# Kernel optimization log

Measured on AMD Instinct MI355X. Metric: run time of the kernel, lower is better.

The kernel has to match this reference:

```python
import jax, jax.numpy as jnp
import numpy as np

H = 768          # hidden_size
NH = 12          # num heads
HD = H // NH     # head dim = 64
FF = 4 * H       # 3072
EPS = 1e-12


def _layer_norm(x, g, b):
    mu = jnp.mean(x, axis=-1, keepdims=True)
    var = jnp.var(x, axis=-1, keepdims=True)
    return (x - mu) * jax.lax.rsqrt(var + EPS) * g + b


def setup_inputs() -> dict:
    key = jax.random.key(0)
    ks = jax.random.split(key, 8)
    B, S = 4, 2048
    s = 0.02
    return {
        "x": jax.random.normal(ks[0], (B, S, H), dtype=jnp.float32),
        "w_qkv": jax.random.normal(ks[1], (H, 3 * H), dtype=jnp.float32) * s,
        "b_qkv": jnp.zeros((3 * H,), dtype=jnp.float32),
        "w_out": jax.random.normal(ks[2], (H, H), dtype=jnp.float32) * s,
        "b_out": jnp.zeros((H,), dtype=jnp.float32),
        "w_ff1": jax.random.normal(ks[3], (H, FF), dtype=jnp.float32) * s,
        "b_ff1": jnp.zeros((FF,), dtype=jnp.float32),
        "w_ff2": jax.random.normal(ks[4], (FF, H), dtype=jnp.float32) * s,
        "b_ff2": jnp.zeros((H,), dtype=jnp.float32),
        "g1": jnp.ones((H,), dtype=jnp.float32),
        "be1": jnp.zeros((H,), dtype=jnp.float32),
        "g2": jnp.ones((H,), dtype=jnp.float32),
        "be2": jnp.zeros((H,), dtype=jnp.float32),
    }


def reference(x, w_qkv, b_qkv, w_out, b_out, w_ff1, b_ff1, w_ff2, b_ff2, g1, be1, g2, be2):
    B, S, _ = x.shape
    qkv = x @ w_qkv + b_qkv                     # [B,S,3H]
    q, k, v = jnp.split(qkv, 3, axis=-1)
    # [B,S,H] -> [B,NH,S,HD]
    def heads(t):
        return t.reshape(B, S, NH, HD).transpose(0, 2, 1, 3)
    q, k, v = heads(q), heads(k), heads(v)
    scores = jnp.einsum("bhqd,bhkd->bhqk", q, k) / np.sqrt(HD).astype(np.float32)
    attn = jax.nn.softmax(scores, axis=-1)      # dropout is identity at inference
    ctx = jnp.einsum("bhqk,bhkd->bhqd", attn, v)
    ctx = ctx.transpose(0, 2, 1, 3).reshape(B, S, H)
    attn_out = ctx @ w_out + b_out
    x1 = _layer_norm(x + attn_out, g1, be1)
    h = jax.nn.gelu(x1 @ w_ff1 + b_ff1, approximate=False)  # torch exact gelu
    ffn = h @ w_ff2 + b_ff2
    return _layer_norm(x1 + ffn, g2, be2)
```

## Files before the change

kernel.cpp:

```cpp
#include <hip/hip_runtime.h>
#include <cstdint>
#include <cstddef>

typedef unsigned short u16;
typedef __attribute__((ext_vector_type(8))) short bf16x8;
typedef __attribute__((ext_vector_type(4))) float f32x4;

__device__ __forceinline__ u16 f2b(float f) {
    union { float f; unsigned u; } un; un.f = f;
    unsigned r = un.u + 0x7fffu + ((un.u >> 16) & 1u);
    return (u16)(r >> 16);
}
__device__ __forceinline__ u16 f2b_trunc(float f) {
    union { float f; unsigned u; } un; un.f = f;
    return (u16)(un.u >> 16);
}
__device__ __forceinline__ float fast_exp2(float x) {
#if __has_builtin(__builtin_amdgcn_exp2f)
    return __builtin_amdgcn_exp2f(x);
#else
    return exp2f(x);
#endif
}

__device__ __forceinline__ void stage16(const u16* g, u16* l) {
    __builtin_amdgcn_global_load_lds(
        (const __attribute__((address_space(1))) void*)g,
        (__attribute__((address_space(3))) void*)l, 16, 0, 0);
}

__global__ __launch_bounds__(256) void cast_bf16_x4(const float* __restrict__ in,
                                                    u16* __restrict__ out, int n4) {
    int i = blockIdx.x * 256 + threadIdx.x;
    if (i >= n4) return;
    float4 v = ((const float4*)in)[i];
    ushort4 o;
    o.x = f2b(v.x); o.y = f2b(v.y); o.z = f2b(v.z); o.w = f2b(v.w);
    ((ushort4*)out)[i] = o;
}

__global__ __launch_bounds__(256) void transpose_cast(const float* __restrict__ in,
                                                      u16* __restrict__ out, int K, int N) {
    __shared__ float t[32][33];
    const int n0 = blockIdx.x * 32, k0 = blockIdx.y * 32;
    const int tx = threadIdx.x, ty = threadIdx.y;
#pragma unroll
    for (int i = 0; i < 4; ++i)
        t[ty + i * 8][tx] = in[(size_t)(k0 + ty + i * 8) * N + n0 + tx];
    __syncthreads();
#pragma unroll
    for (int i = 0; i < 4; ++i)
        out[(size_t)(n0 + ty + i * 8) * K + k0 + tx] = f2b(t[tx][ty + i * 8]);
}

template <int EPI>
__global__ __launch_bounds__(256, 3)
void gemm_bf16(const u16* __restrict__ A, const u16* __restrict__ BT,
               const float* __restrict__ bias,
               void* __restrict__ outp, u16* __restrict__ vt, int M, int N, int K) {
    __shared__ __align__(16) u16 Ash[128 * 64];
    __shared__ __align__(16) u16 Bsh[128 * 64];
    const int m0 = blockIdx.y * 128, n0 = blockIdx.x * 128;
    const int tid = threadIdx.x;
    const int w = tid >> 6, lane = tid & 63;
    const int l16 = lane & 15, quad = lane >> 4;
    const int wm = (w >> 1) * 64, wn = (w & 1) * 64;

    const int srow = lane >> 3;
    const int sgrp = (lane & 7) ^ (srow & 7);
    const int xk = l16 & 7;

    const f32x4 vzero = {0.f, 0.f, 0.f, 0.f};
    f32x4 acc[4][4];
#pragma unroll
    for (int i = 0; i < 4; ++i)
#pragma unroll
        for (int j = 0; j < 4; ++j) acc[i][j] = vzero;

    for (int k0 = 0; k0 < K; k0 += 64) {
#pragma unroll
        for (int it = 0; it < 4; ++it) {
            const int c = it * 4 + w;
            const int r = c * 8 + srow;
            stage16(A + (size_t)(m0 + r) * K + k0 + sgrp * 8, &Ash[c * 512 + lane * 8]);
        }
#pragma unroll
        for (int it = 0; it < 4; ++it) {
            const int c = it * 4 + w;
            const int r = c * 8 + srow;
            stage16(BT + (size_t)(n0 + r) * K + k0 + sgrp * 8, &Bsh[c * 512 + lane * 8]);
        }
        __syncthreads();

        bf16x8 af[4][2], bfr[4][2];
#pragma unroll
        for (int mt = 0; mt < 4; ++mt)
#pragma unroll
            for (int s = 0; s < 2; ++s)
                af[mt][s] = *(const bf16x8*)&Ash[(wm + mt * 16 + l16) * 64 +
                                                 (((s << 2) + quad) ^ xk) * 8];
#pragma unroll
        for (int nt = 0; nt < 4; ++nt)
#pragma unroll
            for (int s = 0; s < 2; ++s)
                bfr[nt][s] = *(const bf16x8*)&Bsh[(wn + nt * 16 + l16) * 64 +
                                                  (((s << 2) + quad) ^ xk) * 8];
#pragma unroll
        for (int mt = 0; mt < 4; ++mt)
#pragma unroll
            for (int nt = 0; nt < 4; ++nt)
#pragma unroll
                for (int s = 0; s < 2; ++s)
                    acc[mt][nt] = __builtin_amdgcn_mfma_f32_16x16x32_bf16(
                        af[mt][s], bfr[nt][s], acc[mt][nt], 0, 0, 0);
        __syncthreads();
    }

    if (EPI == 3 && n0 >= 1536) {
#pragma unroll
        for (int mt = 0; mt < 4; ++mt) {
#pragma unroll
            for (int nt = 0; nt < 4; ++nt) {
                const int col = n0 + wn + nt * 16 + l16;
                const int c = col - 1536;
                const int h = c >> 6, d = c & 63;
                const float bv = bias[col];
                const int row0 = m0 + wm + mt * 16 + quad * 4;
                const int b = row0 >> 11, tok = row0 & 2047;
                ushort4 o;
                o.x = f2b(acc[mt][nt][0] + bv);
                o.y = f2b(acc[mt][nt][1] + bv);
                o.z = f2b(acc[mt][nt][2] + bv);
                o.w = f2b(acc[mt][nt][3] + bv);
                *(ushort4*)&vt[(size_t)(((b * 12 + h) << 6) + d) * 2048 + tok] = o;
            }
        }
        return;
    }

#pragma unroll
    for (int mt = 0; mt < 4; ++mt) {
#pragma unroll
        for (int nt = 0; nt < 4; ++nt) {
            const int col = n0 + wn + nt * 16 + l16;
            const float bv = bias[col];
#pragma unroll
            for (int r = 0; r < 4; ++r) {
                const int row = m0 + wm + mt * 16 + quad * 4 + r;
                float v = acc[mt][nt][r] + bv;
                if (EPI == 2) {
                    v = 0.5f * v * (1.f + erff(v * 0.70710678118654752f));
                    ((u16*)outp)[(size_t)row * N + col] = f2b(v);
                } else {
                    ((u16*)outp)[(size_t)row * N + col] = f2b(v);
                }
            }
        }
    }
}

__global__ __launch_bounds__(256, 4)
void gemm_bf16_r64(const u16* __restrict__ A, const u16* __restrict__ BT,
                   const float* __restrict__ bias, const float* __restrict__ resid,
                   float* __restrict__ outp, int M, int N, int K) {
    __shared__ __align__(16) u16 Ash[64 * 64];
    __shared__ __align__(16) u16 Bsh[128 * 64];
    const int m0 = blockIdx.y * 64, n0 = blockIdx.x * 128;
    const int tid = threadIdx.x;
    const int w = tid >> 6, lane = tid & 63;
    const int l16 = lane & 15, quad = lane >> 4;
    const int wm = (w >> 1) * 32, wn = (w & 1) * 64;

    const int srow = lane >> 3;
    const int sgrp = (lane & 7) ^ (srow & 7);
    const int xk = l16 & 7;

    const f32x4 vzero = {0.f, 0.f, 0.f, 0.f};
    f32x4 acc[2][4];
#pragma unroll
    for (int i = 0; i < 2; ++i)
#pragma unroll
        for (int j = 0; j < 4; ++j) acc[i][j] = vzero;

    for (int k0 = 0; k0 < K; k0 += 64) {
#pragma unroll
        for (int it = 0; it < 2; ++it) {
            const int c = it * 4 + w;
            const int r = c * 8 + srow;
            stage16(A + (size_t)(m0 + r) * K + k0 + sgrp * 8, &Ash[c * 512 + lane * 8]);
        }
#pragma unroll
        for (int it = 0; it < 4; ++it) {
            const int c = it * 4 + w;
            const int r = c * 8 + srow;
            stage16(BT + (size_t)(n0 + r) * K + k0 + sgrp * 8, &Bsh[c * 512 + lane * 8]);
        }
        __syncthreads();

        bf16x8 af[2][2], bfr[4][2];
#pragma unroll
        for (int mt = 0; mt < 2; ++mt)
#pragma unroll
            for (int s = 0; s < 2; ++s)
                af[mt][s] = *(const bf16x8*)&Ash[(wm + mt * 16 + l16) * 64 +
                                                 (((s << 2) + quad) ^ xk) * 8];
#pragma unroll
        for (int nt = 0; nt < 4; ++nt)
#pragma unroll
            for (int s = 0; s < 2; ++s)
                bfr[nt][s] = *(const bf16x8*)&Bsh[(wn + nt * 16 + l16) * 64 +
                                                  (((s << 2) + quad) ^ xk) * 8];
#pragma unroll
        for (int mt = 0; mt < 2; ++mt)
#pragma unroll
            for (int nt = 0; nt < 4; ++nt)
#pragma unroll
                for (int s = 0; s < 2; ++s)
                    acc[mt][nt] = __builtin_amdgcn_mfma_f32_16x16x32_bf16(
                        af[mt][s], bfr[nt][s], acc[mt][nt], 0, 0, 0);
        __syncthreads();
    }

#pragma unroll
    for (int mt = 0; mt < 2; ++mt) {
#pragma unroll
        for (int nt = 0; nt < 4; ++nt) {
            const int col = n0 + wn + nt * 16 + l16;
            const float bv = bias[col];
#pragma unroll
            for (int r = 0; r < 4; ++r) {
                const int row = m0 + wm + mt * 16 + quad * 4 + r;
                outp[(size_t)row * N + col] =
                    acc[mt][nt][r] + bv + resid[(size_t)row * N + col];
            }
        }
    }
}

__global__ __launch_bounds__(256, 4)
void attn_fused(const u16* __restrict__ qkv, const u16* __restrict__ vt,
                u16* __restrict__ ctx) {
    constexpr int LDP = 68;
    __shared__ __align__(16) u16 Ksh[64 * 64];
    __shared__ __align__(16) u16 Vsh[64 * 64];
    __shared__ __align__(16) short Psh[4 * 32 * LDP];

    const int q0 = blockIdx.x * 128;
    const int h = blockIdx.y, b = blockIdx.z;
    const int tid = threadIdx.x;
    const int w = tid >> 6, lane = tid & 63, l16 = lane & 15, quad = lane >> 4;
    short* Pw = Psh + w * 32 * LDP;

    const int srow = lane >> 3;
    const int sgrp = (lane & 7) ^ (srow & 7);
    const int xk = l16 & 7;

    const u16* Qp = qkv + (size_t)b * 2048 * 2304 + h * 64;
    const u16* Kp = Qp + 768;
    const u16* Vtp = vt + ((size_t)(b * 12 + h) << 6) * 2048;

    bf16x8 qf[2][2];
#pragma unroll
    for (int mt = 0; mt < 2; ++mt)
#pragma unroll
        for (int s = 0; s < 2; ++s)
            qf[mt][s] = *(const bf16x8*)(Qp +
                (size_t)(q0 + w * 32 + mt * 16 + l16) * 2304 + s * 32 + quad * 8);

    const f32x4 vzero = {0.f, 0.f, 0.f, 0.f};
    f32x4 oacc[2][4];
    float l_r[2][4];
#pragma unroll
    for (int mt = 0; mt < 2; ++mt) {
#pragma unroll
        for (int dt = 0; dt < 4; ++dt) oacc[mt][dt] = vzero;
#pragma unroll
        for (int r = 0; r < 4; ++r) l_r[mt][r] = 0.f;
    }

    constexpr float SCALE = 0.18033688011112042f;

    for (int kt = 0; kt < 2048; kt += 64) {
#pragma unroll
        for (int it = 0; it < 2; ++it) {
            const int c = it * 4 + w;
            const int r = c * 8 + srow;
            stage16(Kp + (size_t)(kt + r) * 2304 + sgrp * 8, &Ksh[c * 512 + lane * 8]);
        }
#pragma unroll
        for (int it = 0; it < 2; ++it) {
            const int c = it * 4 + w;
            const int r = c * 8 + srow;
            stage16(Vtp + (size_t)r * 2048 + kt + sgrp * 8, &Vsh[c * 512 + lane * 8]);
        }
        __syncthreads();

        bf16x8 kfr[4][2];
#pragma unroll
        for (int nt = 0; nt < 4; ++nt)
#pragma unroll
            for (int s = 0; s < 2; ++s)
                kfr[nt][s] = *(const bf16x8*)&Ksh[(nt * 16 + l16) * 64 +
                                                  (((s << 2) + quad) ^ xk) * 8];

        f32x4 sacc[2][4];
#pragma unroll
        for (int mt = 0; mt < 2; ++mt)
#pragma unroll
            for (int nt = 0; nt < 4; ++nt) {
                sacc[mt][nt] = vzero;
#pragma unroll
                for (int s = 0; s < 2; ++s)
                    sacc[mt][nt] = __builtin_amdgcn_mfma_f32_16x16x32_bf16(
                        qf[mt][s], kfr[nt][s], sacc[mt][nt], 0, 0, 0);
            }

#pragma unroll
        for (int mt = 0; mt < 2; ++mt) {
#pragma unroll
            for (int r = 0; r < 4; ++r) {
                float p0 = fast_exp2(sacc[mt][0][r] * SCALE);
                float p1 = fast_exp2(sacc[mt][1][r] * SCALE);
                float p2 = fast_exp2(sacc[mt][2][r] * SCALE);
                float p3 = fast_exp2(sacc[mt][3][r] * SCALE);
                l_r[mt][r] += (p0 + p1) + (p2 + p3);
                short* prow = &Pw[(mt * 16 + quad * 4 + r) * LDP + l16];
                prow[0]  = (short)f2b_trunc(p0);
                prow[16] = (short)f2b_trunc(p1);
                prow[32] = (short)f2b_trunc(p2);
                prow[48] = (short)f2b_trunc(p3);
            }
        }

        bf16x8 vfr[4][2];
#pragma unroll
        for (int dt = 0; dt < 4; ++dt)
#pragma unroll
            for (int s = 0; s < 2; ++s)
                vfr[dt][s] = *(const bf16x8*)&Vsh[(dt * 16 + l16) * 64 +
                                                  (((s << 2) + quad) ^ xk) * 8];

#pragma unroll
        for (int mt = 0; mt < 2; ++mt) {
            bf16x8 pf[2];
#pragma unroll
            for (int s = 0; s < 2; ++s) {
                union { struct { short4 lo, hi; } h2; bf16x8 v; } u;
                const short* base = &Pw[(mt * 16 + l16) * LDP + s * 32 + quad * 8];
                u.h2.lo = *(const short4*)(base);
                u.h2.hi = *(const short4*)(base + 4);
                pf[s] = u.v;
            }
#pragma unroll
            for (int dt = 0; dt < 4; ++dt)
#pragma unroll
                for (int s = 0; s < 2; ++s)
                    oacc[mt][dt] = __builtin_amdgcn_mfma_f32_16x16x32_bf16(
                        pf[s], vfr[dt][s], oacc[mt][dt], 0, 0, 0);
        }
        __syncthreads();
    }

#pragma unroll
    for (int mt = 0; mt < 2; ++mt)
#pragma unroll
        for (int r = 0; r < 4; ++r) {
#pragma unroll
            for (int off = 1; off < 16; off <<= 1)
                l_r[mt][r] += __shfl_xor(l_r[mt][r], off);
            l_r[mt][r] = 1.f / l_r[mt][r];
        }

#pragma unroll
    for (int mt = 0; mt < 2; ++mt)
#pragma unroll
        for (int dt = 0; dt < 4; ++dt)
#pragma unroll
            for (int r = 0; r < 4; ++r) {
                const int row = q0 + w * 32 + mt * 16 + quad * 4 + r;
                ctx[(size_t)(b * 2048 + row) * 768 + h * 64 + dt * 16 + l16] =
                    f2b(oacc[mt][dt][r] * l_r[mt][r]);
            }
}

template <bool WB>
__global__ __launch_bounds__(256)
void layernorm_k(const float* __restrict__ y, const float* __restrict__ g,
                 const float* __restrict__ be, float* __restrict__ outf,
                 u16* __restrict__ outb) {
    const int row = blockIdx.x;
    const int tid = threadIdx.x;
    const float* yr = y + (size_t)row * 768;
    float v[3], s = 0.f, s2 = 0.f;
#pragma unroll
    for (int i = 0; i < 3; ++i) {
        float x = yr[tid + i * 256];
        v[i] = x; s += x; s2 += x * x;
    }
#pragma unroll
    for (int off = 32; off >= 1; off >>= 1) {
        s += __shfl_xor(s, off);
        s2 += __shfl_xor(s2, off);
    }
    __shared__ float red[2][4];
    const int w = tid >> 6;
    if ((tid & 63) == 0) { red[0][w] = s; red[1][w] = s2; }
    __syncthreads();
    s = red[0][0] + red[0][1] + red[0][2] + red[0][3];
    s2 = red[1][0] + red[1][1] + red[1][2] + red[1][3];
    const float mu = s * (1.f / 768.f);
    const float var = s2 * (1.f / 768.f) - mu * mu;
    const float rs = rsqrtf(var + 1e-12f);
#pragma unroll
    for (int i = 0; i < 3; ++i) {
        const int c = tid + i * 256;
        const float o = (v[i] - mu) * rs * g[c] + be[c];
        outf[(size_t)row * 768 + c] = o;
        if (WB) outb[(size_t)row * 768 + c] = f2b(o);
    }
}

extern "C" void kernel_launch(void* const* d_in, const int* in_sizes, int n_in,
                              void* d_out, int out_size, void* d_ws, size_t ws_size,
                              hipStream_t stream) {
    const float* x    = (const float*)d_in[0];
    const float* wqkv = (const float*)d_in[1];
    const float* bqkv = (const float*)d_in[2];
    const float* wout = (const float*)d_in[3];
    const float* bout = (const float*)d_in[4];
    const float* wff1 = (const float*)d_in[5];
    const float* bff1 = (const float*)d_in[6];
    const float* wff2 = (const float*)d_in[7];
    const float* bff2 = (const float*)d_in[8];
    const float* g1   = (const float*)d_in[9];
    const float* be1  = (const float*)d_in[10];
    const float* g2   = (const float*)d_in[11];
    const float* be2  = (const float*)d_in[12];

    char* ws = (char*)d_ws;
    constexpr size_t o_xb    = 0;
    constexpr size_t o_wqkvT = o_xb    + (size_t)8192 * 768 * 2;
    constexpr size_t o_woutT = o_wqkvT + (size_t)2304 * 768 * 2;
    constexpr size_t o_wff1T = o_woutT + (size_t)768 * 768 * 2;
    constexpr size_t o_wff2T = o_wff1T + (size_t)3072 * 768 * 2;
    constexpr size_t o_qkv   = o_wff2T + (size_t)768 * 3072 * 2;
    constexpr size_t o_ctx   = o_qkv   + (size_t)8192 * 2304 * 2;
    constexpr size_t o_y     = o_ctx   + (size_t)8192 * 768 * 2;
    constexpr size_t o_x1f   = o_y     + (size_t)8192 * 768 * 4;
    constexpr size_t o_x1b   = o_x1f   + (size_t)8192 * 768 * 4;
    constexpr size_t o_h     = o_qkv;
    constexpr size_t o_vt    = o_x1b;

    u16*   xb    = (u16*)(ws + o_xb);
    u16*   wqkvT = (u16*)(ws + o_wqkvT);
    u16*   woutT = (u16*)(ws + o_woutT);
    u16*   wff1T = (u16*)(ws + o_wff1T);
    u16*   wff2T = (u16*)(ws + o_wff2T);
    u16*   qkvb  = (u16*)(ws + o_qkv);
    u16*   ctxb  = (u16*)(ws + o_ctx);
    float* y     = (float*)(ws + o_y);
    float* x1f   = (float*)(ws + o_x1f);
    u16*   x1b   = (u16*)(ws + o_x1b);
    u16*   hb    = (u16*)(ws + o_h);
    u16*   vt    = (u16*)(ws + o_vt);

    cast_bf16_x4<<<(8192 * 768 / 4 + 255) / 256, 256, 0, stream>>>(x, xb, 8192 * 768 / 4);
    transpose_cast<<<dim3(2304 / 32, 768 / 32),  dim3(32, 8), 0, stream>>>(wqkv, wqkvT, 768, 2304);
    transpose_cast<<<dim3(768 / 32,  768 / 32),  dim3(32, 8), 0, stream>>>(wout, woutT, 768, 768);
    transpose_cast<<<dim3(3072 / 32, 768 / 32),  dim3(32, 8), 0, stream>>>(wff1, wff1T, 768, 3072);
    transpose_cast<<<dim3(768 / 32,  3072 / 32), dim3(32, 8), 0, stream>>>(wff2, wff2T, 3072, 768);

    gemm_bf16<3><<<dim3(2304 / 128, 8192 / 128), 256, 0, stream>>>(
        xb, wqkvT, bqkv, qkvb, vt, 8192, 2304, 768);

    attn_fused<<<dim3(2048 / 128, 12, 4), 256, 0, stream>>>(qkvb, vt, ctxb);

    gemm_bf16_r64<<<dim3(768 / 128, 8192 / 64), 256, 0, stream>>>(
        ctxb, woutT, bout, x, y, 8192, 768, 768);

    layernorm_k<true><<<8192, 256, 0, stream>>>(y, g1, be1, x1f, x1b);

    gemm_bf16<2><<<dim3(3072 / 128, 8192 / 128), 256, 0, stream>>>(
        x1b, wff1T, bff1, hb, nullptr, 8192, 3072, 768);

    gemm_bf16_r64<<<dim3(768 / 128, 8192 / 64), 256, 0, stream>>>(
        hb, wff2T, bff2, x1f, y, 8192, 768, 3072);

    layernorm_k<false><<<8192, 256, 0, stream>>>(y, g2, be2, (float*)d_out, nullptr);
}
```

Measured before the change: 388.4 us.

## Split attention over key halves with combine kernel; store residual intermediates in bf16

Attention now runs over two halves of the key range in separate blocks, which doubles the grid. Each block writes unnormalized f32 partial outputs and row sums, and a new combine kernel adds them and normalizes into bf16 ctx. The goal is to fill more CUs, since the original 768-block grid underused the GPU. The cost is extra f32 global traffic for the partials plus one more launch. Separately, the pre-layernorm sums y and the residual x1 are now stored in bf16 instead of f32 to cut memory traffic, at some cost in precision.

Result: slower. 403.2 us (+3.8%).

```diff
diff --git a/kernel.cpp b/kernel.cpp
--- a/kernel.cpp
+++ b/kernel.cpp
@@ -14,6 +14,10 @@
 __device__ __forceinline__ u16 f2b_trunc(float f) {
     union { float f; unsigned u; } un; un.f = f;
     return (u16)(un.u >> 16);
+}
+__device__ __forceinline__ float b2f(u16 h) {
+    union { unsigned u; float f; } un; un.u = ((unsigned)h) << 16;
+    return un.f;
 }
 __device__ __forceinline__ float fast_exp2(float x) {
 #if __has_builtin(__builtin_amdgcn_exp2f)
@@ -159,10 +163,11 @@
     }
 }
 
+template <bool RESF32>
 __global__ __launch_bounds__(256, 4)
 void gemm_bf16_r64(const u16* __restrict__ A, const u16* __restrict__ BT,
-                   const float* __restrict__ bias, const float* __restrict__ resid,
-                   float* __restrict__ outp, int M, int N, int K) {
+                   const float* __restrict__ bias, const void* __restrict__ resid,
+                   u16* __restrict__ outp, int M, int N, int K) {
     __shared__ __align__(16) u16 Ash[64 * 64];
     __shared__ __align__(16) u16 Bsh[128 * 64];
     const int m0 = blockIdx.y * 64, n0 = blockIdx.x * 128;
@@ -230,8 +235,10 @@
 #pragma unroll
             for (int r = 0; r < 4; ++r) {
                 const int row = m0 + wm + mt * 16 + quad * 4 + r;
-                outp[(size_t)row * N + col] =
-                    acc[mt][nt][r] + bv + resid[(size_t)row * N + col];
+                const size_t idx = (size_t)row * N + col;
+                const float rv = RESF32 ? ((const float*)resid)[idx]
+                                        : b2f(((const u16*)resid)[idx]);
+                outp[idx] = f2b(acc[mt][nt][r] + bv + rv);
             }
         }
     }
@@ -239,17 +246,20 @@
 
 __global__ __launch_bounds__(256, 4)
 void attn_fused(const u16* __restrict__ qkv, const u16* __restrict__ vt,
-                u16* __restrict__ ctx) {
+                float* __restrict__ O0, float* __restrict__ O1,
+                float* __restrict__ lbuf) {
     constexpr int LDP = 68;
     __shared__ __align__(16) u16 Ksh[64 * 64];
     __shared__ __align__(16) u16 Vsh[64 * 64];
     __shared__ __align__(16) short Psh[4 * 32 * LDP];
 
     const int q0 = blockIdx.x * 128;
-    const int h = blockIdx.y, b = blockIdx.z;
+    const int h = blockIdx.y;
+    const int b = blockIdx.z >> 1, half = blockIdx.z & 1;
     const int tid = threadIdx.x;
     const int w = tid >> 6, lane = tid & 63, l16 = lane & 15, quad = lane >> 4;
     short* Pw = Psh + w * 32 * LDP;
+    float* Op = half ? O1 : O0;
 
     const int srow = lane >> 3;
     const int sgrp = (lane & 7) ^ (srow & 7);
@@ -279,8 +289,9 @@
     }
 
     constexpr float SCALE = 0.18033688011112042f;
-
-    for (int kt = 0; kt < 2048; kt += 64) {
+    const int kt0 = half * 1024;
+
+    for (int kt = kt0; kt < kt0 + 1024; kt += 64) {
 #pragma unroll
         for (int it = 0; it < 2; ++it) {
             const int c = it * 4 + w;
@@ -364,12 +375,19 @@
 #pragma unroll
     for (int mt = 0; mt < 2; ++mt)
 #pragma unroll
-        for (int r = 0; r < 4; ++r) {
+        for (int r = 0; r < 4; ++r)
 #pragma unroll
             for (int off = 1; off < 16; off <<= 1)
                 l_r[mt][r] += __shfl_xor(l_r[mt][r], off);
-            l_r[mt][r] = 1.f / l_r[mt][r];
-        }
+
+    if (l16 == 0) {
+        float* lb = lbuf + ((size_t)((half * 4 + b) * 12 + h)) * 2048;
+#pragma unroll
+        for (int mt = 0; mt < 2; ++mt)
+#pragma unroll
+            for (int r = 0; r < 4; ++r)
+                lb[q0 + w * 32 + mt * 16 + quad * 4 + r] = l_r[mt][r];
+    }
 
 #pragma unroll
     for (int mt = 0; mt < 2; ++mt)
@@ -378,23 +396,43 @@
 #pragma unroll
             for (int r = 0; r < 4; ++r) {
                 const int row = q0 + w * 32 + mt * 16 + quad * 4 + r;
-                ctx[(size_t)(b * 2048 + row) * 768 + h * 64 + dt * 16 + l16] =
-                    f2b(oacc[mt][dt][r] * l_r[mt][r]);
-            }
-}
-
-template <bool WB>
+                Op[(size_t)(b * 2048 + row) * 768 + h * 64 + dt * 16 + l16] =
+                    oacc[mt][dt][r];
+            }
+}
+
+__global__ __launch_bounds__(192)
+void attn_combine(const float* __restrict__ O0, const float* __restrict__ O1,
+                  const float* __restrict__ lbuf, u16* __restrict__ ctx) {
+    const int r = blockIdx.x;
+    const int tid = threadIdx.x;
+    const int b = r >> 11, q = r & 2047;
+    const int h = tid >> 4;
+    const float l0 = lbuf[((size_t)(b * 12 + h)) * 2048 + q];
+    const float l1 = lbuf[((size_t)((4 + b) * 12 + h)) * 2048 + q];
+    const float inv = 1.f / (l0 + l1);
+    const float4 a = ((const float4*)O0)[(size_t)r * 192 + tid];
+    const float4 c = ((const float4*)O1)[(size_t)r * 192 + tid];
+    ushort4 o;
+    o.x = f2b((a.x + c.x) * inv);
+    o.y = f2b((a.y + c.y) * inv);
+    o.z = f2b((a.z + c.z) * inv);
+    o.w = f2b((a.w + c.w) * inv);
+    ((ushort4*)ctx)[(size_t)r * 192 + tid] = o;
+}
+
+template <bool OUTF32>
 __global__ __launch_bounds__(256)
-void layernorm_k(const float* __restrict__ y, const float* __restrict__ g,
+void layernorm_k(const u16* __restrict__ y, const float* __restrict__ g,
                  const float* __restrict__ be, float* __restrict__ outf,
                  u16* __restrict__ outb) {
     const int row = blockIdx.x;
     const int tid = threadIdx.x;
-    const float* yr = y + (size_t)row * 768;
+    const u16* yr = y + (size_t)row * 768;
     float v[3], s = 0.f, s2 = 0.f;
 #pragma unroll
     for (int i = 0; i < 3; ++i) {
-        float x = yr[tid + i * 256];
+        float x = b2f(yr[tid + i * 256]);
         v[i] = x; s += x; s2 += x * x;
     }
 #pragma unroll
@@ -415,8 +453,8 @@
     for (int i = 0; i < 3; ++i) {
         const int c = tid + i * 256;
         const float o = (v[i] - mu) * rs * g[c] + be[c];
-        outf[(size_t)row * 768 + c] = o;
-        if (WB) outb[(size_t)row * 768 + c] = f2b(o);
+        if (OUTF32) outf[(size_t)row * 768 + c] = o;
+        else        outb[(size_t)row * 768 + c] = f2b(o);
     }
 }
 
@@ -450,6 +488,7 @@
     constexpr size_t o_x1b   = o_x1f   + (size_t)8192 * 768 * 4;
     constexpr size_t o_h     = o_qkv;
     constexpr size_t o_vt    = o_x1b;
+    constexpr size_t o_l     = o_wqkvT;
 
     u16*   xb    = (u16*)(ws + o_xb);
     u16*   wqkvT = (u16*)(ws + o_wqkvT);
@@ -458,11 +497,13 @@
     u16*   wff2T = (u16*)(ws + o_wff2T);
     u16*   qkvb  = (u16*)(ws + o_qkv);
     u16*   ctxb  = (u16*)(ws + o_ctx);
-    float* y     = (float*)(ws + o_y);
-    float* x1f   = (float*)(ws + o_x1f);
+    float* O0    = (float*)(ws + o_y);
+    float* O1    = (float*)(ws + o_x1f);
+    u16*   yb    = (u16*)(ws + o_y);
     u16*   x1b   = (u16*)(ws + o_x1b);
     u16*   hb    = (u16*)(ws + o_h);
     u16*   vt    = (u16*)(ws + o_vt);
+    float* lbuf  = (float*)(ws + o_l);
 
     cast_bf16_x4<<<(8192 * 768 / 4 + 255) / 256, 256, 0, stream>>>(x, xb, 8192 * 768 / 4);
     transpose_cast<<<dim3(2304 / 32, 768 / 32),  dim3(32, 8), 0, stream>>>(wqkv, wqkvT, 768, 2304);
@@ -473,18 +514,19 @@
     gemm_bf16<3><<<dim3(2304 / 128, 8192 / 128), 256, 0, stream>>>(
         xb, wqkvT, bqkv, qkvb, vt, 8192, 2304, 768);
 
-    attn_fused<<<dim3(2048 / 128, 12, 4), 256, 0, stream>>>(qkvb, vt, ctxb);
-
-    gemm_bf16_r64<<<dim3(768 / 128, 8192 / 64), 256, 0, stream>>>(
-        ctxb, woutT, bout, x, y, 8192, 768, 768);
-
-    layernorm_k<true><<<8192, 256, 0, stream>>>(y, g1, be1, x1f, x1b);
+    attn_fused<<<dim3(2048 / 128, 12, 8), 256, 0, stream>>>(qkvb, vt, O0, O1, lbuf);
+    attn_combine<<<8192, 192, 0, stream>>>(O0, O1, lbuf, ctxb);
+
+    gemm_bf16_r64<true><<<dim3(768 / 128, 8192 / 64), 256, 0, stream>>>(
+        ctxb, woutT, bout, x, yb, 8192, 768, 768);
+
+    layernorm_k<false><<<8192, 256, 0, stream>>>(yb, g1, be1, nullptr, x1b);
 
     gemm_bf16<2><<<dim3(3072 / 128, 8192 / 128), 256, 0, stream>>>(
         x1b, wff1T, bff1, hb, nullptr, 8192, 3072, 768);
 
-    gemm_bf16_r64<<<dim3(768 / 128, 8192 / 64), 256, 0, stream>>>(
-        hb, wff2T, bff2, x1f, y, 8192, 768, 3072);
-
-    layernorm_k<false><<<8192, 256, 0, stream>>>(y, g2, be2, (float*)d_out, nullptr);
-}
+    gemm_bf16_r64<false><<<dim3(768 / 128, 8192 / 64), 256, 0, stream>>>(
+        hb, wff2T, bff2, x1b, yb, 8192, 768, 3072);
+
+    layernorm_k<true><<<8192, 256, 0, stream>>>(yb, g2, be2, (float*)d_out, nullptr);
+}
```
